# Optimization experiments

Measured on AMD Instinct MI355X. Metric: run time of the kernel, lower is better.

Reference implementation:

```python
import jax, jax.numpy as jnp
import numpy as np
import math

STRIDE = 32
CTR_CLAMP = 32.0
SCALE_CLAMP = math.log(1000.0 / 16)  # DEFAULT_SCALE_CLAMP
CONF_THRESH = 0.05
NMS_THRESH = 0.6
TOPK = 1000
NUM_CLASSES = 80
CLASS_OFFSET = 1.0e5  # separates classes so one IoU pass == per-class NMS


def setup_inputs() -> dict:
    key = jax.random.key(0)
    k1, k2 = jax.random.split(key)
    fmp_h, fmp_w = 100, 100
    A = 5
    M = fmp_h * fmp_w * A  # 50000 candidates
    cls_pred = jax.random.normal(k1, (M, NUM_CLASSES), dtype=jnp.float32)
    reg_pred = jax.random.normal(k2, (M, 4), dtype=jnp.float32)
    anchor_size = jnp.array([[32, 32], [64, 64], [128, 128], [256, 256], [512, 512]], dtype=jnp.float32)
    return {"cls_pred": cls_pred, "reg_pred": reg_pred, "anchor_size": anchor_size,
            "fmp_h": fmp_h, "fmp_w": fmp_w}


def _generate_anchors(anchor_size, fmp_h, fmp_w):
    # anchors laid out as [H*W, A, 4] -> [M, 4], matching torch.meshgrid order
    ys, xs = jnp.meshgrid(jnp.arange(fmp_h, dtype=jnp.float32),
                          jnp.arange(fmp_w, dtype=jnp.float32), indexing="ij")
    xy = (jnp.stack([xs, ys], axis=-1).reshape(-1, 2) + 0.5) * STRIDE  # [HW, 2]
    A = anchor_size.shape[0]
    anchor_xy = jnp.repeat(xy[:, None, :], A, axis=1)                   # [HW, A, 2]
    anchor_wh = jnp.broadcast_to(anchor_size[None], (xy.shape[0], A, 2))
    return jnp.concatenate([anchor_xy, anchor_wh], axis=-1).reshape(-1, 4)  # [M, 4]


def _decode_boxes(anchors, reg):
    # anchors/reg: [K, 4] (cx, cy, w, h) / (dx, dy, dw, dh)
    ctr_off = jnp.clip(reg[:, :2] * anchors[:, 2:], -CTR_CLAMP, CTR_CLAMP)
    ctr_xy = anchors[:, :2] + ctr_off
    wh = anchors[:, 2:] * jnp.exp(jnp.minimum(reg[:, 2:], SCALE_CLAMP))
    return jnp.concatenate([ctr_xy - 0.5 * wh, ctr_xy + 0.5 * wh], axis=-1)  # x1y1x2y2


def _greedy_nms_keep(boxes, valid):
    # boxes: [K, 4] already score-sorted descending; valid: [K] bool
    x1, y1, x2, y2 = boxes[:, 0], boxes[:, 1], boxes[:, 2], boxes[:, 3]
    areas = (x2 - x1) * (y2 - y1)
    xx1 = jnp.maximum(x1[:, None], x1[None, :])
    yy1 = jnp.maximum(y1[:, None], y1[None, :])
    xx2 = jnp.minimum(x2[:, None], x2[None, :])
    yy2 = jnp.minimum(y2[:, None], y2[None, :])
    inter = jnp.maximum(1e-28, xx2 - xx1) * jnp.maximum(1e-28, yy2 - yy1)
    iou = inter / (areas[:, None] + areas[None, :] - inter + 1e-14)  # [K, K]
    idxs = jnp.arange(boxes.shape[0])

    def body(i, keep):
        suppress = keep[i] & (iou[i] > NMS_THRESH) & (idxs > i)
        return keep & ~suppress

    return jax.lax.fori_loop(0, boxes.shape[0], body, valid)


def reference(cls_pred, reg_pred, anchor_size, fmp_h, fmp_w):
    anchors = _generate_anchors(anchor_size, fmp_h, fmp_w)  # [M, 4]
    probs = jax.nn.sigmoid(cls_pred)                        # [M, C]
    scores = probs.max(axis=-1)
    labels = probs.argmax(axis=-1)
    # top-k candidates (lax.top_k returns scores sorted descending)
    scores, idx = jax.lax.top_k(scores, TOPK)
    labels = labels[idx]
    reg = reg_pred[idx]
    anc = anchors[idx]
    boxes = _decode_boxes(anc, reg)                         # [K, 4] in pixels
    valid = scores >= CONF_THRESH
    # per-class NMS via class offsets (boxes of different classes never overlap)
    boxes_off = boxes + labels.astype(boxes.dtype)[:, None] * CLASS_OFFSET
    keep = _greedy_nms_keep(boxes_off, valid)
    img_w = fmp_w * STRIDE
    img_h = fmp_h * STRIDE
    scale = jnp.array([img_w, img_h, img_w, img_h], dtype=boxes.dtype)
    nboxes = jnp.clip(boxes / scale, 0.0, 1.0)
    m = keep.astype(boxes.dtype)
    return nboxes * m[:, None], scores * m, jnp.where(keep, labels, -1), keep
```

## Files before the change

kernel.cpp:

```cpp
#include <hip/hip_runtime.h>
#include <math.h>

#define NCLS 80
#define TOPK 1000
#define CAND_CAP 4096
#define TRI_IDX(f, g) ((f) * 16 - ((f) * ((f) - 1)) / 2 + ((g) - (f)))

__device__ __forceinline__ float sigmoid_np(float x) {
  float e = (float)exp(-(double)x);
  return 1.0f / (1.0f + e);
}
__device__ __forceinline__ float exp_np(float x) { return (float)exp((double)x); }

__device__ __forceinline__ unsigned fkey(float s) {
  unsigned u = __float_as_uint(s);
  return ((int)u < 0) ? ~u : (u | 0x80000000u);
}

#define KEY_BASE 0xBF000000u
__device__ __forceinline__ unsigned kbin(unsigned key) { return (key >> 11) & 0xFFFu; }

__device__ __forceinline__ void agg_add(unsigned* h, unsigned bin, bool pred) {
  unsigned long long rem = __ballot(pred);
  const int lane = threadIdx.x & 63;
  while (rem) {
    int leader = __ffsll(rem) - 1;
    unsigned lb = (unsigned)__shfl((int)bin, leader, 64);
    unsigned long long m = __ballot(pred && bin == lb);
    if (lane == leader) atomicAdd(&h[lb], (unsigned)__popcll(m));
    rem &= ~m;
  }
}

__global__ void k_zero(unsigned* __restrict__ p, int nwords) {
  int i = blockIdx.x * 256 + threadIdx.x;
  if (i < nwords) p[i] = 0u;
}

__launch_bounds__(1024)
__global__ void k_score(const float* __restrict__ cls, float* __restrict__ scores,
                        int* __restrict__ labels, unsigned* __restrict__ ghist1, int M) {
  __shared__ unsigned h1[4096];
  const int t = threadIdx.x;
  #pragma unroll
  for (int k = 0; k < 4; ++k) h1[t + 1024 * k] = 0u;
  __syncthreads();

  int gid = blockIdx.x * 1024 + t;
  int anchor = gid >> 2;
  int q = gid & 3;
  bool act = anchor < M;
  float lv[20];
  float best = -3.4e38f; int bc = 0;
  if (act) {
    const float4* row = reinterpret_cast<const float4*>(cls) + (size_t)anchor * (NCLS / 4);
    #pragma unroll
    for (int k = 0; k < 5; ++k) {
      float4 v = row[q + 4 * k];
      int cbase = (q + 4 * k) * 4;
      lv[4 * k + 0] = v.x; lv[4 * k + 1] = v.y; lv[4 * k + 2] = v.z; lv[4 * k + 3] = v.w;
      if (v.x > best) { best = v.x; bc = cbase + 0; }
      if (v.y > best) { best = v.y; bc = cbase + 1; }
      if (v.z > best) { best = v.z; bc = cbase + 2; }
      if (v.w > best) { best = v.w; bc = cbase + 3; }
    }
  } else {
    #pragma unroll
    for (int k = 0; k < 20; ++k) lv[k] = -3.4e38f;
  }
  #pragma unroll
  for (int d = 1; d < 4; d <<= 1) {
    float ob = __shfl_xor(best, d, 64);
    int oc = __shfl_xor(bc, d, 64);
    if (ob > best || (ob == best && oc < bc)) { best = ob; bc = oc; }
  }
  float s = sigmoid_np(best);
  float sp = s * (1.0f - s);
  float band = (s < 1.0f && sp > 0.0f) ? (4.8e-7f / sp) : 3.4e38f;
  float thresh = best - band;
  int cclose = 1 << 30;
  #pragma unroll
  for (int k = 0; k < 5; ++k) {
    #pragma unroll
    for (int j = 0; j < 4; ++j) {
      int c = (q + 4 * k) * 4 + j;
      if (lv[4 * k + j] >= thresh && c < cclose) cclose = c;
    }
  }
  #pragma unroll
  for (int d = 1; d < 4; d <<= 1) {
    int oc = __shfl_xor(cclose, d, 64);
    if (oc < cclose) cclose = oc;
  }
  int lab = bc;
  if (act && cclose < bc && q == 0) {
    float bp = -1.0f; int bl = 0;
    for (int c = 0; c < NCLS; ++c) {
      float p = sigmoid_np(cls[(size_t)anchor * NCLS + c]);
      if (p > bp) { bp = p; bl = c; }
    }
    lab = bl;
  }
  unsigned key = fkey(s);
  if (act && q == 0) {
    scores[anchor] = s;
    labels[anchor] = lab;
  }
  agg_add(h1, kbin(key), act && q == 0 && key >= KEY_BASE);
  __syncthreads();
  #pragma unroll
  for (int k = 0; k < 4; ++k) {
    unsigned c = h1[t + 1024 * k];
    if (c) atomicAdd(&ghist1[t + 1024 * k], c);
  }
}

__launch_bounds__(1024)
__global__ void k_cr(const unsigned* __restrict__ ghist1, const float* __restrict__ scores,
                     unsigned long long* __restrict__ cand, unsigned* __restrict__ gcount,
                     unsigned* __restrict__ done,
                     const int* __restrict__ labels, const float* __restrict__ reg,
                     const float* __restrict__ asz, const int* __restrict__ pW,
                     int M, int A,
                     float* __restrict__ sel_score, int* __restrict__ sel_label,
                     float* __restrict__ boxes, float* __restrict__ areas,
                     float* __restrict__ obox) {
  __shared__ unsigned chunks[1024];
  __shared__ unsigned long long ck[CAND_CAP];
  __shared__ int sB1;
  __shared__ unsigned wcnt[16];
  __shared__ unsigned sbase;
  __shared__ bool sLast;
  const int t = threadIdx.x;
  const int lane = t & 63, wid = t >> 6;
  if (t == 0) sB1 = 0;

  unsigned hb0 = ghist1[4 * t], hb1 = ghist1[4 * t + 1],
           hb2 = ghist1[4 * t + 2], hb3 = ghist1[4 * t + 3];
  chunks[t] = hb0 + hb1 + hb2 + hb3;
  __syncthreads();
  for (int d = 1; d < 1024; d <<= 1) {
    unsigned v = chunks[t] + ((t + d < 1024) ? chunks[t + d] : 0u);
    __syncthreads(); chunks[t] = v; __syncthreads();
  }
  {
    unsigned ssc = chunks[t];
    unsigned ssn = (t + 1 < 1024) ? chunks[t + 1] : 0u;
    if (ssc >= (unsigned)TOPK && ssn < (unsigned)TOPK) {
      unsigned hb[4] = {hb0, hb1, hb2, hb3};
      unsigned run = ssn;
      for (int b = 3; b >= 0; --b) {
        run += hb[b];
        if (run >= (unsigned)TOPK) { sB1 = 4 * t + b; break; }
      }
    }
  }
  __syncthreads();
  const unsigned T = KEY_BASE + ((unsigned)sB1 << 11);

  int base = (blockIdx.x * 1024 + t) * 4;
  unsigned keys[4]; int idxs[4]; int np = 0;
  if (base + 3 < M) {
    float4 v = *reinterpret_cast<const float4*>(scores + base);
    unsigned kk[4] = {fkey(v.x), fkey(v.y), fkey(v.z), fkey(v.w)};
    #pragma unroll
    for (int j = 0; j < 4; ++j)
      if (kk[j] >= T) { keys[np] = kk[j]; idxs[np] = base + j; ++np; }
  } else {
    for (int i = base; i < M; ++i) {
      unsigned key = fkey(scores[i]);
      if (key >= T) { keys[np] = key; idxs[np] = i; ++np; }
    }
  }
  int sc = np;
  #pragma unroll
  for (int d = 1; d < 64; d <<= 1) {
    int o = __shfl_up(sc, d, 64);
    if (lane >= d) sc += o;
  }
  if (lane == 63) wcnt[wid] = (unsigned)sc;
  __syncthreads();
  if (t == 0) {
    unsigned acc = 0;
    for (int w = 0; w < 16; ++w) { unsigned v = wcnt[w]; wcnt[w] = acc; acc += v; }
    sbase = acc ? atomicAdd(gcount, acc) : 0u;
  }
  __syncthreads();
  unsigned pos = sbase + wcnt[wid] + (unsigned)(sc - np);
  for (int j = 0; j < np; ++j) {
    if (pos < (unsigned)CAND_CAP)
      cand[pos] = ((unsigned long long)keys[j] << 32) | (unsigned)(~(unsigned)idxs[j]);
    ++pos;
  }

  __threadfence();
  __syncthreads();
  if (t == 0) sLast = (atomicAdd(done, 1u) == (unsigned)(gridDim.x - 1));
  __syncthreads();
  if (!sLast) return;
  __threadfence();

  unsigned n = *gcount; if (n > (unsigned)CAND_CAP) n = (unsigned)CAND_CAP;
  for (int i = t; i < (int)n; i += 1024) ck[i] = cand[i];
  __syncthreads();
  for (int cc = 0; cc < CAND_CAP; cc += 1024) {
    if ((unsigned)cc >= n) break;
    int c = cc + t;
    bool actv = (unsigned)c < n;
    unsigned long long my = actv ? ck[c] : 0ull;
    int r = 0;
    for (int j = 0; j < (int)n; ++j) r += (ck[j] > my);
    if (actv && r < TOPK) {
      unsigned key = (unsigned)(my >> 32);
      unsigned u = (key & 0x80000000u) ? (key ^ 0x80000000u) : ~key;
      float scv = __uint_as_float(u);
      int idx = (int)(~(unsigned)my);
      int lab = labels[idx];
      int W = *pW;
      int a = idx % A;
      int cell = idx / A;
      int x = cell % W;
      int y = cell / W;
      float aw = asz[a * 2 + 0], ah = asz[a * 2 + 1];
      float ax = ((float)x + 0.5f) * 32.0f;
      float ay = ((float)y + 0.5f) * 32.0f;
      float4 rg = *reinterpret_cast<const float4*>(reg + (size_t)idx * 4);
      float offx = fminf(fmaxf(rg.x * aw, -32.0f), 32.0f);
      float offy = fminf(fmaxf(rg.y * ah, -32.0f), 32.0f);
      float cx = ax + offx, cy = ay + offy;
      const float SC = 4.135166556742356f;
      float bw = aw * exp_np(fminf(rg.z, SC));
      float bh = ah * exp_np(fminf(rg.w, SC));
      float x1 = cx - 0.5f * bw, y1 = cy - 0.5f * bh;
      float x2 = cx + 0.5f * bw, y2 = cy + 0.5f * bh;
      float off = (float)lab * 100000.0f;
      float ox1 = x1 + off, oy1 = y1 + off, ox2 = x2 + off, oy2 = y2 + off;
      sel_score[r] = scv; sel_label[r] = lab;
      boxes[r * 4 + 0] = x1; boxes[r * 4 + 1] = y1;
      boxes[r * 4 + 2] = x2; boxes[r * 4 + 3] = y2;
      obox[0 * 1024 + r] = ox1; obox[1 * 1024 + r] = oy1;
      obox[2 * 1024 + r] = ox2; obox[3 * 1024 + r] = oy2;
      areas[r] = (ox2 - ox1) * (oy2 - oy1);
    }
  }
}

union MnLds {
  struct { float so0[1024], so1[1024], so2[1024], so3[1024], sa[1024]; } m;
  struct { unsigned long long sm[8704]; float ssc[1024];
           int pf[136], pg[136]; unsigned long long kwS[16]; } n;
};

__launch_bounds__(1024)
__global__ void k_mn(const float* __restrict__ obox, const float* __restrict__ areas,
                     unsigned long long* __restrict__ maskC, unsigned* __restrict__ done,
                     const float* __restrict__ sel_score, const int* __restrict__ sel_label,
                     const float* __restrict__ boxes,
                     const int* __restrict__ pW, const int* __restrict__ pH,
                     float* __restrict__ out) {
  __shared__ MnLds L;
  __shared__ bool sLast;
  const int t = threadIdx.x;
  const int lane = t & 63;
  const int c = blockIdx.x, j = t;

  L.m.so0[t] = obox[t];        L.m.so1[t] = obox[1024 + t];
  L.m.so2[t] = obox[2048 + t]; L.m.so3[t] = obox[3072 + t];
  L.m.sa[t] = areas[t];
  __syncthreads();
  {
    unsigned long long bits = 0ull;
    if (j < TOPK) {
      float x1j = L.m.so0[j], y1j = L.m.so1[j], x2j = L.m.so2[j], y2j = L.m.so3[j];
      float aj = L.m.sa[j];
      int i0 = c * 64;
      for (int ii = 0; ii < 64; ++ii) {
        int i = i0 + ii;
        if (i < TOPK && i < j) {
          float xx1 = fmaxf(L.m.so0[i], x1j);
          float yy1 = fmaxf(L.m.so1[i], y1j);
          float xx2 = fminf(L.m.so2[i], x2j);
          float yy2 = fminf(L.m.so3[i], y2j);
          float inter = fmaxf(1e-28f, xx2 - xx1) * fmaxf(1e-28f, yy2 - yy1);
          float uni = L.m.sa[i] + aj - inter + 1e-14f;
          float iou = inter / uni;
          if (iou > 0.6f) bits |= (1ull << ii);
        }
      }
    }
    maskC[c * 1024 + j] = bits;
  }

  __threadfence();
  __syncthreads();
  if (t == 0) sLast = (atomicAdd(done, 1u) == (unsigned)(gridDim.x - 1));
  __syncthreads();
  if (!sLast) return;
  __threadfence();
  __syncthreads();

  if (t < 136) {
    int p = t, f = 0;
    while (p >= 16 - f) { p -= 16 - f; ++f; }
    L.n.pf[t] = f; L.n.pg[t] = f + p;
  }
  L.n.ssc[t] = (t < TOPK) ? sel_score[t] : 0.0f;
  __syncthreads();
  for (int i = t; i < 136 * 64; i += 1024) {
    int p = i >> 6, l = i & 63;
    L.n.sm[i] = maskC[L.n.pf[p] * 1024 + L.n.pg[p] * 64 + l];
  }
  __syncthreads();

  if (t < 64) {
    unsigned long long supp[16];
    #pragma unroll
    for (int f = 0; f < 16; ++f) supp[f] = 0ull;
    #pragma unroll
    for (int f = 0; f < 16; ++f) {
      unsigned long long ct = L.n.sm[TRI_IDX(f, f) * 64 + lane];
      int r = f * 64 + lane;
      unsigned long long valid = __ballot((r < TOPK) && (L.n.ssc[r] >= 0.05f));
      unsigned long long sup_any = __ballot(ct != 0ull);
      unsigned long long avail = valid & ~supp[f];
      unsigned long long kwf = 0ull;
      while (avail) {
        unsigned long long fs = avail & sup_any;
        if (!fs) { kwf |= avail; break; }
        int i = __ffsll((long long)fs) - 1;
        unsigned long long below = (1ull << i) - 1ull;
        kwf |= avail & below;
        kwf |= (1ull << i);
        unsigned long long vict = __ballot(((ct >> i) & 1ull) != 0ull);
        avail &= ~vict;
        avail &= ~(below | (1ull << i));
      }
      if (lane == 0) L.n.kwS[f] = kwf;
      #pragma unroll
      for (int g = f + 1; g < 16; ++g)
        supp[g] |= __ballot((L.n.sm[TRI_IDX(f, g) * 64 + lane] & kwf) != 0ull);
    }
  }
  __syncthreads();

  float sw = (float)(*pW * 32);
  float sh = (float)(*pH * 32);
  const float4* b4 = reinterpret_cast<const float4*>(boxes);
  if (t < TOPK) {
    int r = t;
    bool kp = (L.n.kwS[r >> 6] >> (r & 63)) & 1ull;
    float m = kp ? 1.0f : 0.0f;
    float4 b = b4[r];
    float b0 = fminf(fmaxf(b.x / sw, 0.0f), 1.0f) * m;
    float b1 = fminf(fmaxf(b.y / sh, 0.0f), 1.0f) * m;
    float b2 = fminf(fmaxf(b.z / sw, 0.0f), 1.0f) * m;
    float b3 = fminf(fmaxf(b.w / sh, 0.0f), 1.0f) * m;
    out[r * 4 + 0] = b0; out[r * 4 + 1] = b1;
    out[r * 4 + 2] = b2; out[r * 4 + 3] = b3;
    out[TOPK * 4 + r] = L.n.ssc[r] * m;
    out[TOPK * 5 + r] = kp ? (float)sel_label[r] : -1.0f;
    out[TOPK * 6 + r] = m;
  }
}

extern "C" void kernel_launch(void* const* d_in, const int* in_sizes, int n_in,
                              void* d_out, int out_size, void* d_ws, size_t ws_size,
                              hipStream_t stream) {
  const float* cls = (const float*)d_in[0];
  const float* reg = (const float*)d_in[1];
  const float* asz = (const float*)d_in[2];
  const int* pH = (const int*)d_in[3];
  const int* pW = (const int*)d_in[4];
  int M = in_sizes[0] / NCLS;
  int A = in_sizes[2] / 2;

  char* ws = (char*)d_ws;
  size_t off = 0;
  auto alloc = [&](size_t bytes) { size_t o = off; off = (off + bytes + 255) & ~(size_t)255; return o; };
  size_t o_h1   = alloc(4096 * sizeof(unsigned));
  size_t o_cnt  = alloc(256);
  size_t zero_end = off;
  size_t o_cand = alloc((size_t)CAND_CAP * sizeof(unsigned long long));
  size_t o_sc   = alloc((size_t)M * sizeof(float));
  size_t o_lb   = alloc((size_t)M * sizeof(int));
  size_t o_ssc  = alloc(1024 * sizeof(float));
  size_t o_slb  = alloc(1024 * sizeof(int));
  size_t o_box  = alloc((size_t)TOPK * 4 * sizeof(float));
  size_t o_area = alloc(1024 * sizeof(float));
  size_t o_obox = alloc(4 * 1024 * sizeof(float));
  size_t o_mask = alloc((size_t)16 * 1024 * sizeof(unsigned long long));
  (void)ws_size; (void)out_size; (void)n_in;

  int zwords = (int)(zero_end / 4);
  k_zero<<<(zwords + 255) / 256, 256, 0, stream>>>((unsigned*)ws, zwords);
  int nblk_score = (M * 4 + 1023) / 1024;
  k_score<<<nblk_score, 1024, 0, stream>>>(
      cls, (float*)(ws + o_sc), (int*)(ws + o_lb), (unsigned*)(ws + o_h1), M);
  int nblk_cmp = ((M + 3) / 4 + 1023) / 1024;
  k_cr<<<nblk_cmp, 1024, 0, stream>>>(
      (const unsigned*)(ws + o_h1), (const float*)(ws + o_sc),
      (unsigned long long*)(ws + o_cand), (unsigned*)(ws + o_cnt),
      (unsigned*)(ws + o_cnt + 4),
      (const int*)(ws + o_lb), reg, asz, pW, M, A,
      (float*)(ws + o_ssc), (int*)(ws + o_slb),
      (float*)(ws + o_box), (float*)(ws + o_area), (float*)(ws + o_obox));
  k_mn<<<16, 1024, 0, stream>>>(
      (const float*)(ws + o_obox), (const float*)(ws + o_area),
      (unsigned long long*)(ws + o_mask), (unsigned*)(ws + o_cnt + 8),
      (const float*)(ws + o_ssc), (const int*)(ws + o_slb),
      (const float*)(ws + o_box), pW, pH, (float*)d_out);
}
```

Before: 86.55 us.

## Merge rank-select and NMS mask into a single-block finalize kernel

Splits the compaction kernel off its last-block tail and moves candidate ranking, box decoding, IoU mask construction, greedy NMS and output writes into one single-block kernel that keeps everything in LDS. This drops the global round-trips for selected boxes, areas and the mask matrix, and removes the last-block atomic handoffs. The IoU mask now covers only upper-triangle tiles, computed by one block instead of 16, which cuts parallelism for the mask phase. The LDS footprint grows to hold all intermediates.

```diff
diff --git a/kernel.cpp b/kernel.cpp
--- a/kernel.cpp
+++ b/kernel.cpp
@@ -116,21 +116,13 @@
 }
 
 __launch_bounds__(1024)
-__global__ void k_cr(const unsigned* __restrict__ ghist1, const float* __restrict__ scores,
-                     unsigned long long* __restrict__ cand, unsigned* __restrict__ gcount,
-                     unsigned* __restrict__ done,
-                     const int* __restrict__ labels, const float* __restrict__ reg,
-                     const float* __restrict__ asz, const int* __restrict__ pW,
-                     int M, int A,
-                     float* __restrict__ sel_score, int* __restrict__ sel_label,
-                     float* __restrict__ boxes, float* __restrict__ areas,
-                     float* __restrict__ obox) {
+__global__ void k_compact(const unsigned* __restrict__ ghist1, const float* __restrict__ scores,
+                          unsigned long long* __restrict__ cand, unsigned* __restrict__ gcount,
+                          int M) {
   __shared__ unsigned chunks[1024];
-  __shared__ unsigned long long ck[CAND_CAP];
   __shared__ int sB1;
   __shared__ unsigned wcnt[16];
   __shared__ unsigned sbase;
-  __shared__ bool sLast;
   const int t = threadIdx.x;
   const int lane = t & 63, wid = t >> 6;
   if (t == 0) sB1 = 0;
@@ -192,24 +184,45 @@
       cand[pos] = ((unsigned long long)keys[j] << 32) | (unsigned)(~(unsigned)idxs[j]);
     ++pos;
   }
-
-  __threadfence();
-  __syncthreads();
-  if (t == 0) sLast = (atomicAdd(done, 1u) == (unsigned)(gridDim.x - 1));
-  __syncthreads();
-  if (!sLast) return;
-  __threadfence();
-
+}
+
+struct FinLds {
+  float so0[1024], so1[1024], so2[1024], so3[1024], sa[1024];
+  float4 bx[1024];
+  float ssc[1024]; int slab[1024];
+  int pf[136], pg[136];
+  unsigned long long kwS[16];
+  union { unsigned long long ck[CAND_CAP]; unsigned long long sm[8704]; } u;
+};
+
+__launch_bounds__(1024)
+__global__ void k_fin(const unsigned long long* __restrict__ cand,
+                      const unsigned* __restrict__ gcount,
+                      const int* __restrict__ labels, const float* __restrict__ reg,
+                      const float* __restrict__ asz, const int* __restrict__ pW,
+                      const int* __restrict__ pH, int A,
+                      float* __restrict__ out) {
+  __shared__ FinLds L;
+  const int t = threadIdx.x;
+  const int lane = t & 63;
+
+  L.ssc[t] = 0.0f;
+  if (t < 136) {
+    int p = t, f = 0;
+    while (p >= 16 - f) { p -= 16 - f; ++f; }
+    L.pf[t] = f; L.pg[t] = f + p;
+  }
   unsigned n = *gcount; if (n > (unsigned)CAND_CAP) n = (unsigned)CAND_CAP;
-  for (int i = t; i < (int)n; i += 1024) ck[i] = cand[i];
-  __syncthreads();
+  for (int i = t; i < (int)n; i += 1024) L.u.ck[i] = cand[i];
+  __syncthreads();
+
   for (int cc = 0; cc < CAND_CAP; cc += 1024) {
     if ((unsigned)cc >= n) break;
     int c = cc + t;
     bool actv = (unsigned)c < n;
-    unsigned long long my = actv ? ck[c] : 0ull;
+    unsigned long long my = actv ? L.u.ck[c] : 0ull;
     int r = 0;
-    for (int j = 0; j < (int)n; ++j) r += (ck[j] > my);
+    for (int j = 0; j < (int)n; ++j) r += (L.u.ck[j] > my);
     if (actv && r < TOPK) {
       unsigned key = (unsigned)(my >> 32);
       unsigned u = (key & 0x80000000u) ? (key ^ 0x80000000u) : ~key;
@@ -235,80 +248,38 @@
       float x2 = cx + 0.5f * bw, y2 = cy + 0.5f * bh;
       float off = (float)lab * 100000.0f;
       float ox1 = x1 + off, oy1 = y1 + off, ox2 = x2 + off, oy2 = y2 + off;
-      sel_score[r] = scv; sel_label[r] = lab;
-      boxes[r * 4 + 0] = x1; boxes[r * 4 + 1] = y1;
-      boxes[r * 4 + 2] = x2; boxes[r * 4 + 3] = y2;
-      obox[0 * 1024 + r] = ox1; obox[1 * 1024 + r] = oy1;
-      obox[2 * 1024 + r] = ox2; obox[3 * 1024 + r] = oy2;
-      areas[r] = (ox2 - ox1) * (oy2 - oy1);
-    }
-  }
-}
-
-union MnLds {
-  struct { float so0[1024], so1[1024], so2[1024], so3[1024], sa[1024]; } m;
-  struct { unsigned long long sm[8704]; float ssc[1024];
-           int pf[136], pg[136]; unsigned long long kwS[16]; } n;
-};
-
-__launch_bounds__(1024)
-__global__ void k_mn(const float* __restrict__ obox, const float* __restrict__ areas,
-                     unsigned long long* __restrict__ maskC, unsigned* __restrict__ done,
-                     const float* __restrict__ sel_score, const int* __restrict__ sel_label,
-                     const float* __restrict__ boxes,
-                     const int* __restrict__ pW, const int* __restrict__ pH,
-                     float* __restrict__ out) {
-  __shared__ MnLds L;
-  __shared__ bool sLast;
-  const int t = threadIdx.x;
-  const int lane = t & 63;
-  const int c = blockIdx.x, j = t;
-
-  L.m.so0[t] = obox[t];        L.m.so1[t] = obox[1024 + t];
-  L.m.so2[t] = obox[2048 + t]; L.m.so3[t] = obox[3072 + t];
-  L.m.sa[t] = areas[t];
-  __syncthreads();
-  {
+      L.ssc[r] = scv; L.slab[r] = lab;
+      L.bx[r] = make_float4(x1, y1, x2, y2);
+      L.so0[r] = ox1; L.so1[r] = oy1; L.so2[r] = ox2; L.so3[r] = oy2;
+      L.sa[r] = (ox2 - ox1) * (oy2 - oy1);
+    }
+  }
+  __syncthreads();
+
+  for (int task = t; task < 136 * 64; task += 1024) {
+    int p = task >> 6, l = task & 63;
+    int f = L.pf[p], g = L.pg[p];
+    int j = g * 64 + l;
     unsigned long long bits = 0ull;
     if (j < TOPK) {
-      float x1j = L.m.so0[j], y1j = L.m.so1[j], x2j = L.m.so2[j], y2j = L.m.so3[j];
-      float aj = L.m.sa[j];
-      int i0 = c * 64;
+      float x1j = L.so0[j], y1j = L.so1[j], x2j = L.so2[j], y2j = L.so3[j];
+      float aj = L.sa[j];
+      int i0 = f * 64;
       for (int ii = 0; ii < 64; ++ii) {
         int i = i0 + ii;
-        if (i < TOPK && i < j) {
-          float xx1 = fmaxf(L.m.so0[i], x1j);
-          float yy1 = fmaxf(L.m.so1[i], y1j);
-          float xx2 = fminf(L.m.so2[i], x2j);
-          float yy2 = fminf(L.m.so3[i], y2j);
+        if (i < TOPK && (f < g || ii < l)) {
+          float xx1 = fmaxf(L.so0[i], x1j);
+          float yy1 = fmaxf(L.so1[i], y1j);
+          float xx2 = fminf(L.so2[i], x2j);
+          float yy2 = fminf(L.so3[i], y2j);
           float inter = fmaxf(1e-28f, xx2 - xx1) * fmaxf(1e-28f, yy2 - yy1);
-          float uni = L.m.sa[i] + aj - inter + 1e-14f;
+          float uni = L.sa[i] + aj - inter + 1e-14f;
           float iou = inter / uni;
           if (iou > 0.6f) bits |= (1ull << ii);
         }
       }
     }
-    maskC[c * 1024 + j] = bits;
-  }
-
-  __threadfence();
-  __syncthreads();
-  if (t == 0) sLast = (atomicAdd(done, 1u) == (unsigned)(gridDim.x - 1));
-  __syncthreads();
-  if (!sLast) return;
-  __threadfence();
-  __syncthreads();
-
-  if (t < 136) {
-    int p = t, f = 0;
-    while (p >= 16 - f) { p -= 16 - f; ++f; }
-    L.n.pf[t] = f; L.n.pg[t] = f + p;
-  }
-  L.n.ssc[t] = (t < TOPK) ? sel_score[t] : 0.0f;
-  __syncthreads();
-  for (int i = t; i < 136 * 64; i += 1024) {
-    int p = i >> 6, l = i & 63;
-    L.n.sm[i] = maskC[L.n.pf[p] * 1024 + L.n.pg[p] * 64 + l];
+    L.u.sm[task] = bits;
   }
   __syncthreads();
 
@@ -318,9 +289,9 @@
     for (int f = 0; f < 16; ++f) supp[f] = 0ull;
     #pragma unroll
     for (int f = 0; f < 16; ++f) {
-      unsigned long long ct = L.n.sm[TRI_IDX(f, f) * 64 + lane];
+      unsigned long long ct = L.u.sm[TRI_IDX(f, f) * 64 + lane];
       int r = f * 64 + lane;
-      unsigned long long valid = __ballot((r < TOPK) && (L.n.ssc[r] >= 0.05f));
+      unsigned long long valid = __ballot((r < TOPK) && (L.ssc[r] >= 0.05f));
       unsigned long long sup_any = __ballot(ct != 0ull);
       unsigned long long avail = valid & ~supp[f];
       unsigned long long kwf = 0ull;
@@ -335,30 +306,29 @@
         avail &= ~vict;
         avail &= ~(below | (1ull << i));
       }
-      if (lane == 0) L.n.kwS[f] = kwf;
+      if (lane == 0) L.kwS[f] = kwf;
       #pragma unroll
       for (int g = f + 1; g < 16; ++g)
-        supp[g] |= __ballot((L.n.sm[TRI_IDX(f, g) * 64 + lane] & kwf) != 0ull);
+        supp[g] |= __ballot((L.u.sm[TRI_IDX(f, g) * 64 + lane] & kwf) != 0ull);
     }
   }
   __syncthreads();
 
   float sw = (float)(*pW * 32);
   float sh = (float)(*pH * 32);
-  const float4* b4 = reinterpret_cast<const float4*>(boxes);
   if (t < TOPK) {
     int r = t;
-    bool kp = (L.n.kwS[r >> 6] >> (r & 63)) & 1ull;
+    bool kp = (L.kwS[r >> 6] >> (r & 63)) & 1ull;
     float m = kp ? 1.0f : 0.0f;
-    float4 b = b4[r];
+    float4 b = L.bx[r];
     float b0 = fminf(fmaxf(b.x / sw, 0.0f), 1.0f) * m;
     float b1 = fminf(fmaxf(b.y / sh, 0.0f), 1.0f) * m;
     float b2 = fminf(fmaxf(b.z / sw, 0.0f), 1.0f) * m;
     float b3 = fminf(fmaxf(b.w / sh, 0.0f), 1.0f) * m;
     out[r * 4 + 0] = b0; out[r * 4 + 1] = b1;
     out[r * 4 + 2] = b2; out[r * 4 + 3] = b3;
-    out[TOPK * 4 + r] = L.n.ssc[r] * m;
-    out[TOPK * 5 + r] = kp ? (float)sel_label[r] : -1.0f;
+    out[TOPK * 4 + r] = L.ssc[r] * m;
+    out[TOPK * 5 + r] = kp ? (float)L.slab[r] : -1.0f;
     out[TOPK * 6 + r] = m;
   }
 }
@@ -383,12 +353,6 @@
   size_t o_cand = alloc((size_t)CAND_CAP * sizeof(unsigned long long));
   size_t o_sc   = alloc((size_t)M * sizeof(float));
   size_t o_lb   = alloc((size_t)M * sizeof(int));
-  size_t o_ssc  = alloc(1024 * sizeof(float));
-  size_t o_slb  = alloc(1024 * sizeof(int));
-  size_t o_box  = alloc((size_t)TOPK * 4 * sizeof(float));
-  size_t o_area = alloc(1024 * sizeof(float));
-  size_t o_obox = alloc(4 * 1024 * sizeof(float));
-  size_t o_mask = alloc((size_t)16 * 1024 * sizeof(unsigned long long));
   (void)ws_size; (void)out_size; (void)n_in;
 
   int zwords = (int)(zero_end / 4);
@@ -397,16 +361,10 @@
   k_score<<<nblk_score, 1024, 0, stream>>>(
       cls, (float*)(ws + o_sc), (int*)(ws + o_lb), (unsigned*)(ws + o_h1), M);
   int nblk_cmp = ((M + 3) / 4 + 1023) / 1024;
-  k_cr<<<nblk_cmp, 1024, 0, stream>>>(
+  k_compact<<<nblk_cmp, 1024, 0, stream>>>(
       (const unsigned*)(ws + o_h1), (const float*)(ws + o_sc),
-      (unsigned long long*)(ws + o_cand), (unsigned*)(ws + o_cnt),
-      (unsigned*)(ws + o_cnt + 4),
-      (const int*)(ws + o_lb), reg, asz, pW, M, A,
-      (float*)(ws + o_ssc), (int*)(ws + o_slb),
-      (float*)(ws + o_box), (float*)(ws + o_area), (float*)(ws + o_obox));
-  k_mn<<<16, 1024, 0, stream>>>(
-      (const float*)(ws + o_obox), (const float*)(ws + o_area),
-      (unsigned long long*)(ws + o_mask), (unsigned*)(ws + o_cnt + 8),
-      (const float*)(ws + o_ssc), (const int*)(ws + o_slb),
-      (const float*)(ws + o_box), pW, pH, (float*)d_out);
-}
+      (unsigned long long*)(ws + o_cand), (unsigned*)(ws + o_cnt), M);
+  k_fin<<<1, 1024, 0, stream>>>(
+      (const unsigned long long*)(ws + o_cand), (const unsigned*)(ws + o_cnt),
+      (const int*)(ws + o_lb), reg, asz, pW, pH, A, (float*)d_out);
+}
```

Result: slower. 178.5 us (+106.2%).
